# Kernel optimization log

Measured on AMD Instinct MI355X. Metric: run time of the kernel, lower is better.

Reference implementation:

```python
import jax, jax.numpy as jnp
import numpy as np
from jax import lax

B, S, T = 16, 256, 800
V, D, M, H = 256, 512, 80, 1024
NH = 4; HD = D // NH; EH = 256  # encoder LSTM hidden per direction


def setup_inputs() -> dict:
    key = jax.random.key(0)
    it = iter(jax.random.split(key, 40))
    def rn(shape, s=0.05):
        return jax.random.normal(next(it), shape, jnp.float32) * s
    return dict(
        text_inputs=jax.random.randint(next(it), (B, S), 0, V),
        mel_targets=jax.random.normal(next(it), (B, T, M), jnp.float32),
        emb=rn((V, D), 0.1),
        conv_w=rn((3, D, D, 5)), conv_b=rn((3, D)),
        bn_gamma=jnp.ones((3, D)), bn_beta=jnp.zeros((3, D)),
        bn_mean=rn((3, D)), bn_var=jnp.ones((3, D)),
        enc_Wih_f=rn((4 * EH, D)), enc_Whh_f=rn((4 * EH, EH)), enc_b_f=rn((4 * EH,)),
        enc_Wih_b=rn((4 * EH, D)), enc_Whh_b=rn((4 * EH, EH)), enc_b_b=rn((4 * EH,)),
        Wq=rn((D, M)), bq=rn((D,)), Wk=rn((D, D)), bk=rn((D,)),
        Wv=rn((D, D)), bv=rn((D,)), Wo=rn((D, D)), bo=rn((D,)),
        dec_Wih1=rn((4 * H, D + M)), dec_b1=rn((4 * H,)),
        dec_Wih2=rn((4 * H, H)), dec_b2=rn((4 * H,)),
        mel_W=rn((M, H)), mel_b=rn((M,)),
        stop_W=rn((1, H)), stop_b=rn((1,)),
    )


def _lstm_cell_zero(x, Wih, b):
    # single-step LSTM cell from zero (h, c); original resets state every timestep
    g = x @ Wih.T + b
    i, f, gg, o = jnp.split(g, 4, axis=-1)
    c = jax.nn.sigmoid(i) * jnp.tanh(gg)  # c0 = 0 -> forget gate contributes nothing
    return jax.nn.sigmoid(o) * jnp.tanh(c)


def _lstm_scan(xs, Wih, Whh, b, hdim, reverse):
    # xs: (S, B, in); PyTorch gate order i,f,g,o
    def step(carry, xt):
        h, c = carry
        g = xt @ Wih.T + h @ Whh.T + b
        i, f, gg, o = jnp.split(g, 4, axis=-1)
        c = jax.nn.sigmoid(f) * c + jax.nn.sigmoid(i) * jnp.tanh(gg)
        h = jax.nn.sigmoid(o) * jnp.tanh(c)
        return (h, c), h
    z = jnp.zeros((xs.shape[1], hdim), xs.dtype)
    _, hs = lax.scan(step, (z, z), xs, reverse=reverse)
    return hs


def reference(text_inputs, mel_targets, emb, conv_w, conv_b, bn_gamma, bn_beta, bn_mean, bn_var, enc_Wih_f, enc_Whh_f, enc_b_f, enc_Wih_b, enc_Whh_b, enc_b_b, Wq, bq, Wk, bk, Wv, bv, Wo, bo, dec_Wih1, dec_b1, dec_Wih2, dec_b2, mel_W, mel_b, stop_W, stop_b):
    b_, t_, m_ = mel_targets.shape
    # ---- encoder ----
    x = emb[text_inputs].transpose(0, 2, 1)  # (B, D, S)
    for i in range(conv_w.shape[0]):
        x = lax.conv_general_dilated(x, conv_w[i], (1,), [(2, 2)], dimension_numbers=('NCH', 'OIH', 'NCH')) + conv_b[i][None, :, None]
        x = bn_gamma[i][None, :, None] * (x - bn_mean[i][None, :, None]) * lax.rsqrt(bn_var[i][None, :, None] + 1e-5) + bn_beta[i][None, :, None]
        x = jax.nn.relu(x)  # dropout in eval mode -> identity
    xs = x.transpose(2, 0, 1)  # (S, B, D)
    hf = _lstm_scan(xs, enc_Wih_f, enc_Whh_f, enc_b_f, EH, False)
    hb = _lstm_scan(xs, enc_Wih_b, enc_Whh_b, enc_b_b, EH, True)
    enc = jnp.concatenate([hf, hb], -1).transpose(1, 0, 2)  # (B, S, D)
    # ---- decoder (teacher forcing): per-step query = previous mel frame ----
    dec_in = jnp.concatenate([jnp.zeros((b_, 1, m_), mel_targets.dtype), mel_targets[:, :-1]], axis=1)  # (B, T, M)
    q = (dec_in @ Wq.T + bq).reshape(b_, t_, NH, HD)
    k = (enc @ Wk.T + bk).reshape(b_, -1, NH, HD)
    v = (enc @ Wv.T + bv).reshape(b_, -1, NH, HD)
    scores = jnp.einsum('bqhd,bkhd->bhqk', q, k) * (1.0 / np.sqrt(HD)).astype(np.float32)
    attn = jax.nn.softmax(scores, axis=-1)
    ctx = jnp.einsum('bhqk,bkhd->bqhd', attn, v).reshape(b_, t_, D) @ Wo.T + bo
    xcat = jnp.concatenate([ctx, dec_in], axis=-1)  # (B, T, D+M)
    # original re-inits decoder LSTM state each timestep -> stateless per-step cells
    h1 = _lstm_cell_zero(xcat, dec_Wih1, dec_b1)
    h2 = _lstm_cell_zero(h1, dec_Wih2, dec_b2)
    mel = h2 @ mel_W.T + mel_b      # (B, T, 80)
    stop = h2 @ stop_W.T + stop_b   # (B, T, 1) - logits (no sigmoid in training path)
    return mel, stop
```

## Files before the change

kernel.cpp:

```cpp
#include <hip/hip_runtime.h>
#include <hip/hip_bf16.h>
#include <math.h>

#define B_ 16
#define S_ 256
#define T_ 800
#define V_ 256
#define D_ 512
#define M_ 80
#define H_ 1024
#define NH_ 4
#define HD_ 128
#define EH_ 256

using bf16x8 = __attribute__((ext_vector_type(8))) short;
using f32x4  = __attribute__((ext_vector_type(4))) float;
typedef _Float16 half8 __attribute__((ext_vector_type(8)));

__device__ __forceinline__ float sigf(float x) { return 1.f / (1.f + __expf(-x)); }
__device__ __forceinline__ float tanhfast(float x) {
    float e = __expf(2.f * x);
    return 1.f - 2.f / (e + 1.f);
}

__device__ __forceinline__ unsigned short f2bf(float f) {
    unsigned int u = __float_as_uint(f);
    unsigned int r = (u + 0x7FFFu + ((u >> 16) & 1u)) >> 16;
    return (unsigned short)r;
}
__device__ __forceinline__ float bf2f(unsigned short u) {
    return __uint_as_float(((unsigned int)u) << 16);
}
__device__ __forceinline__ unsigned short h2u(_Float16 x) {
    union { _Float16 f; unsigned short u; } c; c.f = x; return c.u;
}

#define LDS_BAR() do {                                        \
    asm volatile("s_waitcnt lgkmcnt(0)" ::: "memory");        \
    __builtin_amdgcn_s_barrier();                             \
    __builtin_amdgcn_sched_barrier(0);                        \
} while (0)

__device__ __forceinline__ void gl_lds16(const unsigned short* g, unsigned short* l) {
    __builtin_amdgcn_global_load_lds((const __attribute__((address_space(1))) void*)g,
                                     (__attribute__((address_space(3))) void*)l, 16, 0, 0);
}

__global__ __launch_bounds__(256) void gemm_mfma(
    const unsigned short* __restrict__ A, const unsigned short* __restrict__ Bw,
    void* __restrict__ Cv, const float* __restrict__ bias,
    int M, int N, int K, int ldc, int epi,
    const float* __restrict__ cb, const float* __restrict__ gam,
    const float* __restrict__ bet, const float* __restrict__ mu,
    const float* __restrict__ va)
{
    __shared__ unsigned short As[4096];
    __shared__ unsigned short Bs[4096];
    const int tid = threadIdx.x, w = tid >> 6, lane = tid & 63;
    const int bm = blockIdx.y * 128, bn = blockIdx.x * 128;
    const int wr = w >> 1, wc = w & 1;

    f32x4 acc[4][4];
#pragma unroll
    for (int m = 0; m < 4; ++m)
#pragma unroll
        for (int n = 0; n < 4; ++n) acc[m][n] = (f32x4){0.f, 0.f, 0.f, 0.f};

    const int r0 = w * 16 + (lane >> 2);
    const int k8 = (lane & 3) * 8;
    const unsigned short* Ag = A + (size_t)(bm + r0) * K + k8;
    const unsigned short* Bg = Bw + (size_t)(bn + r0) * K + k8;
    unsigned short* Al = As + w * 512;
    unsigned short* Bl = Bs + w * 512;

    for (int k0 = 0; k0 < K; k0 += 32) {
        __syncthreads();
        gl_lds16(Ag + k0, Al);
        gl_lds16(Ag + (size_t)64 * K + k0, Al + 2048);
        gl_lds16(Bg + k0, Bl);
        gl_lds16(Bg + (size_t)64 * K + k0, Bl + 2048);
        __syncthreads();
        bf16x8 a[4], b[4];
#pragma unroll
        for (int m = 0; m < 4; ++m)
            a[m] = *(const bf16x8*)(As + (wr * 64 + m * 16 + (lane & 15)) * 32 + (lane >> 4) * 8);
#pragma unroll
        for (int n = 0; n < 4; ++n)
            b[n] = *(const bf16x8*)(Bs + (wc * 64 + n * 16 + (lane & 15)) * 32 + (lane >> 4) * 8);
#pragma unroll
        for (int m = 0; m < 4; ++m)
#pragma unroll
            for (int n = 0; n < 4; ++n)
                acc[m][n] = __builtin_amdgcn_mfma_f32_16x16x32_bf16(a[m], b[n], acc[m][n], 0, 0, 0);
    }

    const int cr = (lane >> 4) * 4, ccol = lane & 15;
#pragma unroll
    for (int m = 0; m < 4; ++m)
#pragma unroll
        for (int n = 0; n < 4; ++n) {
            const int col = bn + wc * 64 + n * 16 + ccol;
            const float bv = (bias && !(epi == 4 && col >= 80)) ? bias[col] : 0.f;
#pragma unroll
            for (int j = 0; j < 4; ++j) {
                const int row = bm + wr * 64 + m * 16 + cr + j;
                float v = acc[m][n][j] + bv;
                if (epi == 1) {
                    float x = v + cb[col];
                    v = fmaxf(0.f, gam[col] * (x - mu[col]) * rsqrtf(va[col] + 1e-5f) + bet[col]);
                }
                if (epi == 2) {
                    ((unsigned short*)Cv)[(size_t)row * ldc + col] = f2bf(v);
                } else if (epi == 3) {
                    const int bb2 = row >> 8, ss = row & 255, hh = col >> 7, dd = col & 127;
                    ((unsigned short*)Cv)[((size_t)(bb2 * 4 + hh) * 128 + dd) * 256 + ss] = f2bf(v);
                } else if (epi == 4) {
                    if (col < 80) ((float*)Cv)[(size_t)row * ldc + col] = v;
                } else {
                    ((float*)Cv)[(size_t)row * ldc + col] = v;
                }
            }
        }
}

__global__ __launch_bounds__(256) void attn_qk(
    const unsigned short* __restrict__ q, const unsigned short* __restrict__ k,
    float* __restrict__ scores)
{
    __shared__ unsigned short As[4096];
    __shared__ unsigned short Bs[4096];
    const int tid = threadIdx.x, w = tid >> 6, lane = tid & 63;
    const int bm = blockIdx.y * 128, bn = blockIdx.x * 128;
    const int z = blockIdx.z, b = z >> 2, h = z & 3;
    const int wr = w >> 1, wc = w & 1;

    const unsigned short* A  = q + ((size_t)b * T_) * 512 + h * 128;
    const unsigned short* Bw = k + ((size_t)b * S_) * 512 + h * 128;

    f32x4 acc[4][4];
#pragma unroll
    for (int m = 0; m < 4; ++m)
#pragma unroll
        for (int n = 0; n < 4; ++n) acc[m][n] = (f32x4){0.f, 0.f, 0.f, 0.f};

    const int r0 = w * 16 + (lane >> 2);
    const int k8 = (lane & 3) * 8;
    const unsigned short* Ag = A + (size_t)(bm + r0) * 512 + k8;
    const unsigned short* Bg = Bw + (size_t)(bn + r0) * 512 + k8;
    unsigned short* Al = As + w * 512;
    unsigned short* Bl = Bs + w * 512;

    for (int k0 = 0; k0 < 128; k0 += 32) {
        __syncthreads();
        gl_lds16(Ag + k0, Al);
        gl_lds16(Ag + (size_t)64 * 512 + k0, Al + 2048);
        gl_lds16(Bg + k0, Bl);
        gl_lds16(Bg + (size_t)64 * 512 + k0, Bl + 2048);
        __syncthreads();
        bf16x8 a[4], bfr[4];
#pragma unroll
        for (int m = 0; m < 4; ++m)
            a[m] = *(const bf16x8*)(As + (wr * 64 + m * 16 + (lane & 15)) * 32 + (lane >> 4) * 8);
#pragma unroll
        for (int n = 0; n < 4; ++n)
            bfr[n] = *(const bf16x8*)(Bs + (wc * 64 + n * 16 + (lane & 15)) * 32 + (lane >> 4) * 8);
#pragma unroll
        for (int m = 0; m < 4; ++m)
#pragma unroll
            for (int n = 0; n < 4; ++n)
                acc[m][n] = __builtin_amdgcn_mfma_f32_16x16x32_bf16(a[m], bfr[n], acc[m][n], 0, 0, 0);
    }

    const int cr = (lane >> 4) * 4, ccol = lane & 15;
#pragma unroll
    for (int m = 0; m < 4; ++m)
#pragma unroll
        for (int n = 0; n < 4; ++n) {
            const int col = bn + wc * 64 + n * 16 + ccol;
#pragma unroll
            for (int j = 0; j < 4; ++j) {
                const int row = bm + wr * 64 + m * 16 + cr + j;
                if (row < T_)
                    scores[((size_t)z * T_ + row) * 256 + col] = acc[m][n][j] * 0.08838834764831843f;
            }
        }
}

__global__ __launch_bounds__(256) void attn_sm(
    const float* __restrict__ scores, unsigned short* __restrict__ probs)
{
    const int row = blockIdx.x * 4 + (threadIdx.x >> 6);
    const int lane = threadIdx.x & 63;
    const float4 v = *(const float4*)(scores + (size_t)row * 256 + lane * 4);
    float m = fmaxf(fmaxf(v.x, v.y), fmaxf(v.z, v.w));
    for (int off = 32; off; off >>= 1) m = fmaxf(m, __shfl_xor(m, off));
    float ex = __expf(v.x - m), ey = __expf(v.y - m), ez = __expf(v.z - m), ew = __expf(v.w - m);
    float sum = ex + ey + ez + ew;
    for (int off = 32; off; off >>= 1) sum += __shfl_xor(sum, off);
    const float inv = 1.f / sum;
    ushort4 o;
    o.x = f2bf(ex * inv); o.y = f2bf(ey * inv); o.z = f2bf(ez * inv); o.w = f2bf(ew * inv);
    *(ushort4*)(probs + (size_t)row * 256 + lane * 4) = o;
}

__global__ __launch_bounds__(256) void attn_pv(
    const unsigned short* __restrict__ probs, const unsigned short* __restrict__ vT,
    unsigned short* __restrict__ ctx)
{
    __shared__ unsigned short As[4096];
    __shared__ unsigned short Bs[4096];
    const int tid = threadIdx.x, w = tid >> 6, lane = tid & 63;
    const int bm = blockIdx.y * 128;
    const int z = blockIdx.z, b = z >> 2, h = z & 3;
    const int wr = w >> 1, wc = w & 1;

    const unsigned short* A  = probs + (size_t)z * T_ * 256;
    const unsigned short* Bw = vT + (size_t)z * 128 * 256;

    f32x4 acc[4][4];
#pragma unroll
    for (int m = 0; m < 4; ++m)
#pragma unroll
        for (int n = 0; n < 4; ++n) acc[m][n] = (f32x4){0.f, 0.f, 0.f, 0.f};

    const int r0 = w * 16 + (lane >> 2);
    const int k8 = (lane & 3) * 8;
    const unsigned short* Ag = A + (size_t)(bm + r0) * 256 + k8;
    const unsigned short* Bg = Bw + (size_t)r0 * 256 + k8;
    unsigned short* Al = As + w * 512;
    unsigned short* Bl = Bs + w * 512;

    for (int k0 = 0; k0 < 256; k0 += 32) {
        __syncthreads();
        gl_lds16(Ag + k0, Al);
        gl_lds16(Ag + (size_t)64 * 256 + k0, Al + 2048);
        gl_lds16(Bg + k0, Bl);
        gl_lds16(Bg + (size_t)64 * 256 + k0, Bl + 2048);
        __syncthreads();
        bf16x8 a[4], bfr[4];
#pragma unroll
        for (int m = 0; m < 4; ++m)
            a[m] = *(const bf16x8*)(As + (wr * 64 + m * 16 + (lane & 15)) * 32 + (lane >> 4) * 8);
#pragma unroll
        for (int n = 0; n < 4; ++n)
            bfr[n] = *(const bf16x8*)(Bs + (wc * 64 + n * 16 + (lane & 15)) * 32 + (lane >> 4) * 8);
#pragma unroll
        for (int m = 0; m < 4; ++m)
#pragma unroll
            for (int n = 0; n < 4; ++n)
                acc[m][n] = __builtin_amdgcn_mfma_f32_16x16x32_bf16(a[m], bfr[n], acc[m][n], 0, 0, 0);
    }

    const int cr = (lane >> 4) * 4, ccol = lane & 15;
#pragma unroll
    for (int m = 0; m < 4; ++m)
#pragma unroll
        for (int n = 0; n < 4; ++n) {
            const int col = wc * 64 + n * 16 + ccol;
#pragma unroll
            for (int j = 0; j < 4; ++j) {
                const int row = bm + wr * 64 + m * 16 + cr + j;
                if (row < T_)
                    ctx[((size_t)b * T_ + row) * 512 + h * 128 + col] = f2bf(acc[m][n][j]);
            }
        }
}

__global__ void embed_k(const int* __restrict__ txt, const float* __restrict__ emb,
                        float* __restrict__ xs)
{
    int idx = blockIdx.x * 256 + threadIdx.x;
    if (idx >= B_ * S_ * D_) return;
    int bs = idx >> 9, dd = idx & 511;
    xs[idx] = emb[(size_t)txt[bs] * D_ + dd];
}

__global__ void im2col_bf(const float* __restrict__ in, unsigned short* __restrict__ out)
{
    int idx = blockIdx.x * 256 + threadIdx.x;
    if (idx >= B_ * S_ * 2560) return;
    int r = idx / 2560, cc = idx % 2560;
    int din = cc / 5, kk = cc % 5;
    int b = r >> 8, s = r & 255;
    int sp = s + kk - 2;
    float v = (sp >= 0 && sp < S_) ? in[((size_t)b * S_ + sp) * D_ + din] : 0.f;
    out[idx] = f2bf(v);
}

__global__ void transp_bf(const float* __restrict__ in, unsigned short* __restrict__ out)
{
    int idx = blockIdx.x * 256 + threadIdx.x;
    if (idx >= B_ * S_ * D_) return;
    int d = idx & 511;
    int sb = idx >> 9;
    int s = sb >> 4, b = sb & 15;
    out[idx] = f2bf(in[((size_t)b * S_ + s) * D_ + d]);
}

__global__ void hist2enc(const _Float16* __restrict__ hist, unsigned short* __restrict__ enc)
{
    int idx = blockIdx.x * 256 + threadIdx.x;
    if (idx >= B_ * S_ * D_) return;
    int d = idx & 511;
    int bs = idx >> 9;
    int b = bs >> 8, s = bs & 255;
    int dir = d >> 8, hid = d & 255;
    enc[idx] = f2bf((float)hist[(((size_t)(dir * 16 + b) * 256 + s) * 256) + hid]);
}

__global__ void cvt_all(
    const float* __restrict__ conv_w, const float* __restrict__ Wih_f,
    const float* __restrict__ Wih_b, const float* __restrict__ Wk,
    const float* __restrict__ Wv, const float* __restrict__ Wq,
    const float* __restrict__ Wo, const float* __restrict__ Wih1,
    const float* __restrict__ Wih2, const float* __restrict__ melW,
    unsigned short* __restrict__ cWc, unsigned short* __restrict__ cWif,
    unsigned short* __restrict__ cWib, unsigned short* __restrict__ cWk,
    unsigned short* __restrict__ cWv, unsigned short* __restrict__ cWq,
    unsigned short* __restrict__ cWo, unsigned short* __restrict__ cW1,
    unsigned short* __restrict__ cW2, unsigned short* __restrict__ cWm)
{
    int idx = blockIdx.x * 256 + threadIdx.x;
    if (idx < 3932160) { cWc[idx] = f2bf(conv_w[idx]); return; }
    idx -= 3932160;
    if (idx < 524288) { cWif[idx] = f2bf(Wih_f[idx]); return; }
    idx -= 524288;
    if (idx < 524288) { cWib[idx] = f2bf(Wih_b[idx]); return; }
    idx -= 524288;
    if (idx < 262144) { cWk[idx] = f2bf(Wk[idx]); return; }
    idx -= 262144;
    if (idx < 262144) { cWv[idx] = f2bf(Wv[idx]); return; }
    idx -= 262144;
    if (idx < 49152) {
        int r = idx / 96, k = idx - r * 96;
        cWq[idx] = (k < 80) ? f2bf(Wq[(size_t)r * 80 + k]) : 0;
        return;
    }
    idx -= 49152;
    if (idx < 262144) { cWo[idx] = f2bf(Wo[idx]); return; }
    idx -= 262144;
    if (idx < 1867776) {
        int n = idx / 608, k = idx - n * 608;
        int orig = (n < 1024) ? n : n + 1024;
        cW1[idx] = (k < 592) ? f2bf(Wih1[(size_t)orig * 592 + k]) : 0;
        return;
    }
    idx -= 1867776;
    if (idx < 3145728) {
        int n = idx >> 10, k = idx & 1023;
        int orig = (n < 1024) ? n : n + 1024;
        cW2[idx] = f2bf(Wih2[(size_t)orig * 1024 + k]);
        return;
    }
    idx -= 3145728;
    if (idx < 131072) {
        int r = idx >> 10, k = idx & 1023;
        cWm[idx] = (r < 80) ? f2bf(melW[(size_t)r * 1024 + k]) : 0;
        return;
    }
}

__global__ void decin_k2(const float* __restrict__ mel, unsigned short* __restrict__ din,
                         unsigned short* __restrict__ xcat)
{
    int idx = blockIdx.x * 256 + threadIdx.x;
    if (idx >= B_ * T_ * 96) return;
    int r = idx / 96, j = idx - r * 96;
    int b = r / T_, t = r - b * T_;
    float v = (j < M_ && t > 0) ? mel[((size_t)b * T_ + t - 1) * M_ + j] : 0.f;
    unsigned short bv = f2bf(v);
    din[(size_t)r * 96 + j] = bv;
    xcat[(size_t)r * 608 + 512 + j] = bv;
}

__global__ void dec_cellb2(const unsigned short* __restrict__ g, const float* __restrict__ b,
                           unsigned short* __restrict__ h, int rows)
{
    int idx = blockIdx.x * 256 + threadIdx.x;
    if (idx >= rows * 512) return;
    int r = idx >> 9, j2 = (idx & 511) * 2;
    const unsigned short* gr = g + (size_t)r * 3072;
    ushort2 vi = *(const ushort2*)(gr + j2);
    ushort2 vg = *(const ushort2*)(gr + 1024 + j2);
    ushort2 vo = *(const ushort2*)(gr + 2048 + j2);
    float i0 = sigf(bf2f(vi.x) + b[j2]),          i1 = sigf(bf2f(vi.y) + b[j2 + 1]);
    float g0 = tanhfast(bf2f(vg.x) + b[2048 + j2]), g1 = tanhfast(bf2f(vg.y) + b[2048 + j2 + 1]);
    float o0 = sigf(bf2f(vo.x) + b[3072 + j2]),   o1 = sigf(bf2f(vo.y) + b[3072 + j2 + 1]);
    ushort2 o;
    o.x = f2bf(o0 * tanhfast(i0 * g0));
    o.y = f2bf(o1 * tanhfast(i1 * g1));
    *(ushort2*)(h + (size_t)r * 1024 + j2) = o;
}

__global__ __launch_bounds__(256) void stop_head(
    const unsigned short* __restrict__ h2, const float* __restrict__ sw,
    const float* __restrict__ sb, float* __restrict__ out)
{
    int row = blockIdx.x * 4 + (threadIdx.x >> 6);
    int lane = threadIdx.x & 63;
    const unsigned short* hr = h2 + (size_t)row * H_;
    float acc = 0.f;
#pragma unroll
    for (int i = 0; i < H_; i += 64) acc += bf2f(hr[i + lane]) * sw[i + lane];
    for (int off = 32; off; off >>= 1) acc += __shfl_xor(acc, off);
    if (lane == 0) out[row] = acc + sb[0];
}

__global__ __launch_bounds__(1024, 4) void lstm_persist8(
    const float* __restrict__ gi_f, const float* __restrict__ gi_b,
    const float* __restrict__ Wf, const float* __restrict__ Wb,
    _Float16* __restrict__ hist,
    unsigned long long* __restrict__ hstage)
{
    const int blk = blockIdx.x;
    const int dir = blk >> 1, half = blk & 1;
    const float* gi = dir ? gi_b : gi_f;
    const float* W  = dir ? Wb : Wf;
    const int tid = threadIdx.x, wid = tid >> 6, lane = tid & 63;
    const int l15 = lane & 15, q = lane >> 4;

    __shared__ _Float16 h_lds[16][264];
    __shared__ float exch[512][17];

    half8 w0[8], w1[8];
    {
        const int gt0 = wid >> 3, hb0 = wid & 7;
        const int gt1 = (wid + 16) >> 3;
        const float* wr0 = W + (size_t)(gt0 * 256 + half * 128 + hb0 * 16 + l15) * 256;
        const float* wr1 = W + (size_t)(gt1 * 256 + half * 128 + hb0 * 16 + l15) * 256;
#pragma unroll
        for (int ks = 0; ks < 8; ++ks) {
            half8 a, b;
#pragma unroll
            for (int j = 0; j < 8; ++j) {
                a[j] = (_Float16)wr0[ks * 32 + q * 8 + j];
                b[j] = (_Float16)wr1[ks * 32 + q * 8 + j];
            }
            w0[ks] = a; w1[ks] = b;
        }
    }
    for (int i = tid; i < 16 * 264; i += 1024) ((_Float16*)h_lds)[i] = (_Float16)0.f;
    for (int i = tid; i < 512 * 17; i += 1024) ((float*)exch)[i] = 0.f;

    const int hid = tid & 127;
    const int ba  = tid >> 7;
    const int bb  = ba + 8;
    const int gh  = half * 128 + hid;
    const int pc  = (half ^ 1) * 128 + hid;
    float c0 = 0.f, c1 = 0.f;

    const int exr0 = (wid >> 3) * 128 + (wid & 7) * 16 + l15;
    const int exr1 = ((wid + 16) >> 3) * 128 + (wid & 7) * 16 + l15;

    const int own_base = ((dir * 2 + half) * 8 + ba) * 128 + hid;
    const int par_base = ((dir * 2 + (half ^ 1)) * 8 + ba) * 128 + hid;

    float gp0[4], gp1[4];
    {
        const int s0 = dir ? 255 : 0;
        const float* g0 = gi + ((size_t)s0 * 16 + ba) * 1024 + gh;
        const float* g1 = gi + ((size_t)s0 * 16 + bb) * 1024 + gh;
#pragma unroll
        for (int g2 = 0; g2 < 4; ++g2) { gp0[g2] = g0[g2 * 256]; gp1[g2] = g1[g2 * 256]; }
    }
    __syncthreads();

    for (int step = 0; step < 255; ++step) {
        const int s = dir ? (255 - step) : step;
        const unsigned int tag = (unsigned int)(step + 1);
        const int slot = (step & 1) * 4096;

        float h0, h1;
        {
            float xi = exch[hid][ba] + gp0[0];
            float xf = exch[128 + hid][ba] + gp0[1];
            float xg = exch[256 + hid][ba] + gp0[2];
            float xo = exch[384 + hid][ba] + gp0[3];
            float ig = sigf(xi), fg = sigf(xf), gg = tanhfast(xg), og = sigf(xo);
            c0 = fg * c0 + ig * gg; h0 = og * tanhfast(c0);
            xi = exch[hid][bb] + gp1[0];
            xf = exch[128 + hid][bb] + gp1[1];
            xg = exch[256 + hid][bb] + gp1[2];
            xo = exch[384 + hid][bb] + gp1[3];
            ig = sigf(xi); fg = sigf(xf); gg = tanhfast(xg); og = sigf(xo);
            c1 = fg * c1 + ig * gg; h1 = og * tanhfast(c1);
        }
        h_lds[ba][gh] = (_Float16)h0;
        h_lds[bb][gh] = (_Float16)h1;
        {
            unsigned int d32 = (unsigned int)h2u((_Float16)h0) |
                               ((unsigned int)h2u((_Float16)h1) << 16);
            unsigned long long wv = ((unsigned long long)tag << 32) | d32;
            __hip_atomic_store(&hstage[slot + own_base], wv,
                               __ATOMIC_RELAXED, __HIP_MEMORY_SCOPE_AGENT);
        }
        hist[(((size_t)(dir * 16 + ba) * 256 + s) * 256) + gh] = (_Float16)h0;
        hist[(((size_t)(dir * 16 + bb) * 256 + s) * 256) + gh] = (_Float16)h1;

        {
            const int s2 = dir ? (254 - step) : (step + 1);
            const float* g0 = gi + ((size_t)s2 * 16 + ba) * 1024 + gh;
            const float* g1 = gi + ((size_t)s2 * 16 + bb) * 1024 + gh;
#pragma unroll
            for (int g2 = 0; g2 < 4; ++g2) { gp0[g2] = g0[g2 * 256]; gp1[g2] = g1[g2 * 256]; }
        }

        {
            unsigned long long pv;
            do {
                pv = __hip_atomic_load(&hstage[slot + par_base],
                                       __ATOMIC_RELAXED, __HIP_MEMORY_SCOPE_AGENT);
            } while ((unsigned int)(pv >> 32) != tag);
            unsigned int d32 = (unsigned int)pv;
            *(unsigned short*)&h_lds[ba][pc] = (unsigned short)(d32 & 0xFFFF);
            *(unsigned short*)&h_lds[bb][pc] = (unsigned short)(d32 >> 16);
        }
        LDS_BAR();

        {
            f32x4 a0 = (f32x4){0.f, 0.f, 0.f, 0.f};
            f32x4 a1 = (f32x4){0.f, 0.f, 0.f, 0.f};
            const _Float16* hrow = &h_lds[l15][0];
#pragma unroll
            for (int ks = 0; ks < 8; ++ks) {
                half8 a = *(const half8*)(hrow + ks * 32 + q * 8);
                a0 = __builtin_amdgcn_mfma_f32_16x16x32_f16(a, w0[ks], a0, 0, 0, 0);
                a1 = __builtin_amdgcn_mfma_f32_16x16x32_f16(a, w1[ks], a1, 0, 0, 0);
            }
            *(f32x4*)&exch[exr0][q * 4] = a0;
            *(f32x4*)&exch[exr1][q * 4] = a1;
        }
        LDS_BAR();
    }

    {
        const int s = dir ? 0 : 255;
        float h0, h1;
        float xi = exch[hid][ba] + gp0[0];
        float xf = exch[128 + hid][ba] + gp0[1];
        float xg = exch[256 + hid][ba] + gp0[2];
        float xo = exch[384 + hid][ba] + gp0[3];
        float ig = sigf(xi), fg = sigf(xf), gg = tanhfast(xg), og = sigf(xo);
        c0 = fg * c0 + ig * gg; h0 = og * tanhfast(c0);
        xi = exch[hid][bb] + gp1[0];
        xf = exch[128 + hid][bb] + gp1[1];
        xg = exch[256 + hid][bb] + gp1[2];
        xo = exch[384 + hid][bb] + gp1[3];
        ig = sigf(xi); fg = sigf(xf); gg = tanhfast(xg); og = sigf(xo);
        c1 = fg * c1 + ig * gg; h1 = og * tanhfast(c1);
        hist[(((size_t)(dir * 16 + ba) * 256 + s) * 256) + gh] = (_Float16)h0;
        hist[(((size_t)(dir * 16 + bb) * 256 + s) * 256) + gh] = (_Float16)h1;
    }
}

static inline void launch_mfma(hipStream_t st, const unsigned short* A, const unsigned short* B,
                               void* C, const float* bias, int M, int N, int K, int ldc, int epi = 0,
                               const float* cb = nullptr, const float* gam = nullptr,
                               const float* bet = nullptr, const float* mu = nullptr,
                               const float* va = nullptr)
{
    dim3 grid(N / 128, M / 128);
    gemm_mfma<<<grid, 256, 0, st>>>(A, B, C, bias, M, N, K, ldc, epi, cb, gam, bet, mu, va);
}

extern "C" void kernel_launch(void* const* d_in, const int* in_sizes, int n_in,
                              void* d_out, int out_size, void* d_ws, size_t ws_size,
                              hipStream_t stream)
{
    const int*   text   = (const int*)d_in[0];
    const float* mel_t  = (const float*)d_in[1];
    const float* emb    = (const float*)d_in[2];
    const float* conv_w = (const float*)d_in[3];
    const float* conv_b = (const float*)d_in[4];
    const float* bn_g   = (const float*)d_in[5];
    const float* bn_b   = (const float*)d_in[6];
    const float* bn_m   = (const float*)d_in[7];
    const float* bn_v   = (const float*)d_in[8];
    const float* Wih_f  = (const float*)d_in[9];
    const float* Whh_f  = (const float*)d_in[10];
    const float* b_f    = (const float*)d_in[11];
    const float* Wih_b  = (const float*)d_in[12];
    const float* Whh_b  = (const float*)d_in[13];
    const float* b_b    = (const float*)d_in[14];
    const float* Wq     = (const float*)d_in[15];
    const float* bq     = (const float*)d_in[16];
    const float* Wk     = (const float*)d_in[17];
    const float* bk     = (const float*)d_in[18];
    const float* Wv     = (const float*)d_in[19];
    const float* bv     = (const float*)d_in[20];
    const float* Wo     = (const float*)d_in[21];
    const float* bo     = (const float*)d_in[22];
    const float* Wih1   = (const float*)d_in[23];
    const float* b1     = (const float*)d_in[24];
    const float* Wih2   = (const float*)d_in[25];
    const float* b2     = (const float*)d_in[26];
    const float* melW   = (const float*)d_in[27];
    const float* melb   = (const float*)d_in[28];
    const float* stopW  = (const float*)d_in[29];
    const float* stopb  = (const float*)d_in[30];
    float* out = (float*)d_out;
    (void)in_sizes; (void)n_in; (void)out_size; (void)ws_size;

    float* ws = (float*)d_ws;
    float* big  = ws;
    float* pool = ws + 13107200;

    unsigned long long* hstage = (unsigned long long*)(ws + 6000000);

    float*          gi_f   = pool + 0;
    float*          gi_b   = pool + 4194304;
    unsigned short* enc_bf = (unsigned short*)(pool + 8388608);
    float*          P0     = pool + 9437184;
    float*          P1     = pool + 11534336;
    unsigned short* xsT    = (unsigned short*)(pool + 13631488);
    _Float16*       hist   = (_Float16*)(pool + 14155776);
    unsigned short* kbf    = (unsigned short*)(pool + 0);
    unsigned short* vT     = (unsigned short*)(pool + 1048576);
    unsigned short* qbf    = (unsigned short*)(pool + 2097152);
    unsigned short* probs  = (unsigned short*)(pool + 9437184);
    unsigned short* dinb   = (unsigned short*)(pool + 16008192);
    unsigned short* ctxb   = (unsigned short*)(pool + 16622592);
    unsigned short* gatesb = (unsigned short*)(pool + 0);
    unsigned short* h2b    = (unsigned short*)big;
    unsigned short* h1b    = (unsigned short*)(big + 4000000);
    unsigned short* xcat   = (unsigned short*)(pool + 19899392);
    float*          WB     = pool + 23790592;
    unsigned short* cWc  = (unsigned short*)(WB + 0);
    unsigned short* cWif = (unsigned short*)(WB + 1966080);
    unsigned short* cWib = (unsigned short*)(WB + 2228224);
    unsigned short* cWk  = (unsigned short*)(WB + 2490368);
    unsigned short* cWv  = (unsigned short*)(WB + 2621440);
    unsigned short* cWq  = (unsigned short*)(WB + 2752512);
    unsigned short* cWo  = (unsigned short*)(WB + 2777088);
    unsigned short* cW1  = (unsigned short*)(WB + 2908160);
    unsigned short* cW2  = (unsigned short*)(WB + 3842048);
    unsigned short* cWm  = (unsigned short*)(WB + 5414912);

    auto ceil256 = [](int n) { return (n + 255) / 256; };

    hipMemsetAsync(hstage, 0, 8192 * 8, stream);

    cvt_all<<<ceil256(10960896), 256, 0, stream>>>(
        conv_w, Wih_f, Wih_b, Wk, Wv, Wq, Wo, Wih1, Wih2, melW,
        cWc, cWif, cWib, cWk, cWv, cWq, cWo, cW1, cW2, cWm);

    embed_k<<<ceil256(B_ * S_ * D_), 256, 0, stream>>>(text, emb, P0);
    float* cin = P0;
    float* cout = P1;
    for (int l = 0; l < 3; ++l) {
        im2col_bf<<<ceil256(B_ * S_ * 2560), 256, 0, stream>>>(cin, (unsigned short*)big);
        launch_mfma(stream, (unsigned short*)big, cWc + (size_t)l * 512 * 2560,
                    cout, nullptr, B_ * S_, 512, 2560, 512, 1,
                    conv_b + l * 512, bn_g + l * 512, bn_b + l * 512, bn_m + l * 512, bn_v + l * 512);
        float* tmp = cin; cin = cout; cout = tmp;
    }
    transp_bf<<<ceil256(B_ * S_ * D_), 256, 0, stream>>>(cin, xsT);

    launch_mfma(stream, xsT, cWif, gi_f, b_f, S_ * B_, 1024, 512, 1024);
    launch_mfma(stream, xsT, cWib, gi_b, b_b, S_ * B_, 1024, 512, 1024);
    lstm_persist8<<<4, 1024, 0, stream>>>(gi_f, gi_b, Whh_f, Whh_b, hist, hstage);
    hist2enc<<<ceil256(B_ * S_ * D_), 256, 0, stream>>>(hist, enc_bf);

    launch_mfma(stream, enc_bf, cWk, kbf, bk, B_ * S_, 512, 512, 512, 2);
    launch_mfma(stream, enc_bf, cWv, vT, bv, B_ * S_, 512, 512, 0, 3);
    decin_k2<<<ceil256(B_ * T_ * 96), 256, 0, stream>>>(mel_t, dinb, xcat);
    launch_mfma(stream, dinb, cWq, qbf, bq, B_ * T_, 512, 96, 512, 2);

    attn_qk<<<dim3(2, 7, 64), 256, 0, stream>>>(qbf, kbf, big);
    attn_sm<<<12800, 256, 0, stream>>>(big, probs);
    attn_pv<<<dim3(1, 7, 64), 256, 0, stream>>>(probs, vT, ctxb);

    launch_mfma(stream, ctxb, cWo, xcat, bo, B_ * T_, 512, 512, 608, 2);

    launch_mfma(stream, xcat, cW1, gatesb, nullptr, B_ * T_, 3072, 608, 3072, 2);
    dec_cellb2<<<ceil256(B_ * T_ * 512), 256, 0, stream>>>(gatesb, b1, h1b, B_ * T_);
    launch_mfma(stream, h1b, cW2, gatesb, nullptr, B_ * T_, 3072, 1024, 3072, 2);
    dec_cellb2<<<ceil256(B_ * T_ * 512), 256, 0, stream>>>(gatesb, b2, h2b, B_ * T_);

    launch_mfma(stream, h2b, cWm, out, melb, B_ * T_, 128, 1024, 80, 4);
    stop_head<<<(B_ * T_) / 4, 256, 0, stream>>>(h2b, stopW, stopb, out + (size_t)B_ * T_ * M_);
}
```

Baseline: 1.622 ms.

## Fuse attention QK with softmax and split LSTM recurrence to overlap peer exchange

The QK score kernel and the separate softmax kernel become one kernel. Each block owns 64 query rows across all 256 keys and does the row max and sum in registers plus a small LDS reduction, so the fp32 score matrix is never written to or read back from global memory. Separately, the persistent encoder LSTM splits its recurrent matmul into a local-half part and a peer-half part. The local-half MFMAs run before spinning on the peer block's hidden-state exchange, which is meant to hide inter-block latency on the serial critical path, at the cost of an extra barrier per step.

New measurement: 1.576 ms. 1.03x faster.

```diff
diff --git a/kernel.cpp b/kernel.cpp
--- a/kernel.cpp
+++ b/kernel.cpp
@@ -34,12 +34,6 @@
 __device__ __forceinline__ unsigned short h2u(_Float16 x) {
     union { _Float16 f; unsigned short u; } c; c.f = x; return c.u;
 }
-
-#define LDS_BAR() do {                                        \
-    asm volatile("s_waitcnt lgkmcnt(0)" ::: "memory");        \
-    __builtin_amdgcn_s_barrier();                             \
-    __builtin_amdgcn_sched_barrier(0);                        \
-} while (0)
 
 __device__ __forceinline__ void gl_lds16(const unsigned short* g, unsigned short* l) {
     __builtin_amdgcn_global_load_lds((const __attribute__((address_space(1))) void*)g,
@@ -123,16 +117,18 @@
         }
 }
 
-__global__ __launch_bounds__(256) void attn_qk(
+__global__ __launch_bounds__(256) void attn_qksm(
     const unsigned short* __restrict__ q, const unsigned short* __restrict__ k,
-    float* __restrict__ scores)
-{
-    __shared__ unsigned short As[4096];
-    __shared__ unsigned short Bs[4096];
-    const int tid = threadIdx.x, w = tid >> 6, lane = tid & 63;
-    const int bm = blockIdx.y * 128, bn = blockIdx.x * 128;
-    const int z = blockIdx.z, b = z >> 2, h = z & 3;
-    const int wr = w >> 1, wc = w & 1;
+    unsigned short* __restrict__ probs)
+{
+    __shared__ unsigned short As[2048];
+    __shared__ unsigned short Bs[8192];
+    __shared__ float redm[64][4];
+    __shared__ float reds[64][4];
+    const int tid = threadIdx.x, wid = tid >> 6, lane = tid & 63;
+    const int l15 = lane & 15, bq = lane >> 4;
+    const int bm = blockIdx.x * 64;
+    const int z = blockIdx.y, b = z >> 2, h = z & 3;
 
     const unsigned short* A  = q + ((size_t)b * T_) * 512 + h * 128;
     const unsigned short* Bw = k + ((size_t)b * S_) * 512 + h * 128;
@@ -143,64 +139,81 @@
 #pragma unroll
         for (int n = 0; n < 4; ++n) acc[m][n] = (f32x4){0.f, 0.f, 0.f, 0.f};
 
-    const int r0 = w * 16 + (lane >> 2);
+    const int r0 = wid * 16 + (lane >> 2);
     const int k8 = (lane & 3) * 8;
-    const unsigned short* Ag = A + (size_t)(bm + r0) * 512 + k8;
-    const unsigned short* Bg = Bw + (size_t)(bn + r0) * 512 + k8;
-    unsigned short* Al = As + w * 512;
-    unsigned short* Bl = Bs + w * 512;
 
     for (int k0 = 0; k0 < 128; k0 += 32) {
         __syncthreads();
-        gl_lds16(Ag + k0, Al);
-        gl_lds16(Ag + (size_t)64 * 512 + k0, Al + 2048);
-        gl_lds16(Bg + k0, Bl);
-        gl_lds16(Bg + (size_t)64 * 512 + k0, Bl + 2048);
+        gl_lds16(A + (size_t)(bm + r0) * 512 + k0 + k8, As + wid * 512);
+        gl_lds16(Bw + (size_t)r0 * 512 + k0 + k8,          Bs + wid * 512);
+        gl_lds16(Bw + (size_t)(64 + r0) * 512 + k0 + k8,   Bs + 2048 + wid * 512);
+        gl_lds16(Bw + (size_t)(128 + r0) * 512 + k0 + k8,  Bs + 4096 + wid * 512);
+        gl_lds16(Bw + (size_t)(192 + r0) * 512 + k0 + k8,  Bs + 6144 + wid * 512);
         __syncthreads();
-        bf16x8 a[4], bfr[4];
+        bf16x8 a[4], bb[4];
 #pragma unroll
         for (int m = 0; m < 4; ++m)
-            a[m] = *(const bf16x8*)(As + (wr * 64 + m * 16 + (lane & 15)) * 32 + (lane >> 4) * 8);
+            a[m] = *(const bf16x8*)(As + (m * 16 + l15) * 32 + bq * 8);
 #pragma unroll
         for (int n = 0; n < 4; ++n)
-            bfr[n] = *(const bf16x8*)(Bs + (wc * 64 + n * 16 + (lane & 15)) * 32 + (lane >> 4) * 8);
+            bb[n] = *(const bf16x8*)(Bs + (wid * 64 + n * 16 + l15) * 32 + bq * 8);
 #pragma unroll
         for (int m = 0; m < 4; ++m)
 #pragma unroll
             for (int n = 0; n < 4; ++n)
-                acc[m][n] = __builtin_amdgcn_mfma_f32_16x16x32_bf16(a[m], bfr[n], acc[m][n], 0, 0, 0);
+                acc[m][n] = __builtin_amdgcn_mfma_f32_16x16x32_bf16(a[m], bb[n], acc[m][n], 0, 0, 0);
     }
 
     const int cr = (lane >> 4) * 4, ccol = lane & 15;
-#pragma unroll
-    for (int m = 0; m < 4; ++m)
-#pragma unroll
-        for (int n = 0; n < 4; ++n) {
-            const int col = bn + wc * 64 + n * 16 + ccol;
-#pragma unroll
-            for (int j = 0; j < 4; ++j) {
-                const int row = bm + wr * 64 + m * 16 + cr + j;
-                if (row < T_)
-                    scores[((size_t)z * T_ + row) * 256 + col] = acc[m][n][j] * 0.08838834764831843f;
+    const float SC = 0.08838834764831843f;
+
+    float lmax[4][4];
+#pragma unroll
+    for (int m = 0; m < 4; ++m)
+#pragma unroll
+        for (int j = 0; j < 4; ++j) {
+            float v = fmaxf(fmaxf(acc[m][0][j], acc[m][1][j]),
+                            fmaxf(acc[m][2][j], acc[m][3][j]));
+#pragma unroll
+            for (int off = 1; off < 16; off <<= 1) v = fmaxf(v, __shfl_xor(v, off));
+            lmax[m][j] = v;
+            if (ccol == 0) redm[m * 16 + cr + j][wid] = v;
+        }
+    __syncthreads();
+    float lsum[4][4];
+#pragma unroll
+    for (int m = 0; m < 4; ++m)
+#pragma unroll
+        for (int j = 0; j < 4; ++j) {
+            const int r = m * 16 + cr + j;
+            float mx = fmaxf(fmaxf(redm[r][0], redm[r][1]), fmaxf(redm[r][2], redm[r][3]));
+            lmax[m][j] = mx;
+            float s = 0.f;
+#pragma unroll
+            for (int n = 0; n < 4; ++n) {
+                float p = __expf((acc[m][n][j] - mx) * SC);
+                acc[m][n][j] = p;
+                s += p;
             }
-        }
-}
-
-__global__ __launch_bounds__(256) void attn_sm(
-    const float* __restrict__ scores, unsigned short* __restrict__ probs)
-{
-    const int row = blockIdx.x * 4 + (threadIdx.x >> 6);
-    const int lane = threadIdx.x & 63;
-    const float4 v = *(const float4*)(scores + (size_t)row * 256 + lane * 4);
-    float m = fmaxf(fmaxf(v.x, v.y), fmaxf(v.z, v.w));
-    for (int off = 32; off; off >>= 1) m = fmaxf(m, __shfl_xor(m, off));
-    float ex = __expf(v.x - m), ey = __expf(v.y - m), ez = __expf(v.z - m), ew = __expf(v.w - m);
-    float sum = ex + ey + ez + ew;
-    for (int off = 32; off; off >>= 1) sum += __shfl_xor(sum, off);
-    const float inv = 1.f / sum;
-    ushort4 o;
-    o.x = f2bf(ex * inv); o.y = f2bf(ey * inv); o.z = f2bf(ez * inv); o.w = f2bf(ew * inv);
-    *(ushort4*)(probs + (size_t)row * 256 + lane * 4) = o;
+#pragma unroll
+            for (int off = 1; off < 16; off <<= 1) s += __shfl_xor(s, off);
+            lsum[m][j] = s;
+            if (ccol == 0) reds[r][wid] = s;
+        }
+    __syncthreads();
+#pragma unroll
+    for (int m = 0; m < 4; ++m)
+#pragma unroll
+        for (int j = 0; j < 4; ++j) {
+            const int r = m * 16 + cr + j;
+            const int row = bm + r;
+            if (row >= T_) continue;
+            const float inv = 1.f / (reds[r][0] + reds[r][1] + reds[r][2] + reds[r][3]);
+#pragma unroll
+            for (int n = 0; n < 4; ++n)
+                probs[((size_t)z * T_ + row) * 256 + wid * 64 + n * 16 + ccol] =
+                    f2bf(acc[m][n][j] * inv);
+        }
 }
 
 __global__ __launch_bounds__(256) void attn_pv(
@@ -406,7 +419,7 @@
     if (lane == 0) out[row] = acc + sb[0];
 }
 
-__global__ __launch_bounds__(1024, 4) void lstm_persist8(
+__global__ __launch_bounds__(1024, 4) void lstm_persist9(
     const float* __restrict__ gi_f, const float* __restrict__ gi_b,
     const float* __restrict__ Wf, const float* __restrict__ Wb,
     _Float16* __restrict__ hist,
@@ -418,25 +431,30 @@
     const float* W  = dir ? Wb : Wf;
     const int tid = threadIdx.x, wid = tid >> 6, lane = tid & 63;
     const int l15 = lane & 15, q = lane >> 4;
+    const int half4 = half * 4, ph4 = (half ^ 1) * 4;
 
     __shared__ _Float16 h_lds[16][264];
     __shared__ float exch[512][17];
 
-    half8 w0[8], w1[8];
+    half8 wOA[4], wPA[4], wOB[4], wPB[4];
     {
         const int gt0 = wid >> 3, hb0 = wid & 7;
         const int gt1 = (wid + 16) >> 3;
         const float* wr0 = W + (size_t)(gt0 * 256 + half * 128 + hb0 * 16 + l15) * 256;
         const float* wr1 = W + (size_t)(gt1 * 256 + half * 128 + hb0 * 16 + l15) * 256;
 #pragma unroll
-        for (int ks = 0; ks < 8; ++ks) {
-            half8 a, b;
+        for (int i = 0; i < 4; ++i) {
+            const int kO = (half4 + i) * 32 + q * 8;
+            const int kP = (ph4 + i) * 32 + q * 8;
+            half8 a, b, c, d;
 #pragma unroll
             for (int j = 0; j < 8; ++j) {
-                a[j] = (_Float16)wr0[ks * 32 + q * 8 + j];
-                b[j] = (_Float16)wr1[ks * 32 + q * 8 + j];
+                a[j] = (_Float16)wr0[kO + j];
+                b[j] = (_Float16)wr0[kP + j];
+                c[j] = (_Float16)wr1[kO + j];
+                d[j] = (_Float16)wr1[kP + j];
             }
-            w0[ks] = a; w1[ks] = b;
+            wOA[i] = a; wPA[i] = b; wOB[i] = c; wPB[i] = d;
         }
     }
     for (int i = tid; i < 16 * 264; i += 1024) ((_Float16*)h_lds)[i] = (_Float16)0.f;
@@ -465,7 +483,7 @@
     }
     __syncthreads();
 
-    for (int step = 0; step < 255; ++step) {
+    for (int step = 0; step < 256; ++step) {
         const int s = dir ? (255 - step) : step;
         const unsigned int tag = (unsigned int)(step + 1);
         const int slot = (step & 1) * 4096;
@@ -485,8 +503,6 @@
             ig = sigf(xi); fg = sigf(xf); gg = tanhfast(xg); og = sigf(xo);
             c1 = fg * c1 + ig * gg; h1 = og * tanhfast(c1);
         }
-        h_lds[ba][gh] = (_Float16)h0;
-        h_lds[bb][gh] = (_Float16)h1;
         {
             unsigned int d32 = (unsigned int)h2u((_Float16)h0) |
                                ((unsigned int)h2u((_Float16)h1) << 16);
@@ -494,62 +510,50 @@
             __hip_atomic_store(&hstage[slot + own_base], wv,
                                __ATOMIC_RELAXED, __HIP_MEMORY_SCOPE_AGENT);
         }
+        h_lds[ba][gh] = (_Float16)h0;
+        h_lds[bb][gh] = (_Float16)h1;
         hist[(((size_t)(dir * 16 + ba) * 256 + s) * 256) + gh] = (_Float16)h0;
         hist[(((size_t)(dir * 16 + bb) * 256 + s) * 256) + gh] = (_Float16)h1;
-
-        {
+        if (step < 255) {
             const int s2 = dir ? (254 - step) : (step + 1);
             const float* g0 = gi + ((size_t)s2 * 16 + ba) * 1024 + gh;
             const float* g1 = gi + ((size_t)s2 * 16 + bb) * 1024 + gh;
 #pragma unroll
             for (int g2 = 0; g2 < 4; ++g2) { gp0[g2] = g0[g2 * 256]; gp1[g2] = g1[g2 * 256]; }
         }
-
-        {
-            unsigned long long pv;
-            do {
-                pv = __hip_atomic_load(&hstage[slot + par_base],
-                                       __ATOMIC_RELAXED, __HIP_MEMORY_SCOPE_AGENT);
-            } while ((unsigned int)(pv >> 32) != tag);
-            unsigned int d32 = (unsigned int)pv;
-            *(unsigned short*)&h_lds[ba][pc] = (unsigned short)(d32 & 0xFFFF);
-            *(unsigned short*)&h_lds[bb][pc] = (unsigned short)(d32 >> 16);
-        }
-        LDS_BAR();
-
-        {
-            f32x4 a0 = (f32x4){0.f, 0.f, 0.f, 0.f};
-            f32x4 a1 = (f32x4){0.f, 0.f, 0.f, 0.f};
+        __syncthreads();
+
+        if (step < 255) {
+            f32x4 acc0 = (f32x4){0.f, 0.f, 0.f, 0.f};
+            f32x4 acc1 = (f32x4){0.f, 0.f, 0.f, 0.f};
             const _Float16* hrow = &h_lds[l15][0];
 #pragma unroll
-            for (int ks = 0; ks < 8; ++ks) {
-                half8 a = *(const half8*)(hrow + ks * 32 + q * 8);
-                a0 = __builtin_amdgcn_mfma_f32_16x16x32_f16(a, w0[ks], a0, 0, 0, 0);
-                a1 = __builtin_amdgcn_mfma_f32_16x16x32_f16(a, w1[ks], a1, 0, 0, 0);
+            for (int i = 0; i < 4; ++i) {
+                half8 a = *(const half8*)(hrow + (half4 + i) * 32 + q * 8);
+                acc0 = __builtin_amdgcn_mfma_f32_16x16x32_f16(a, wOA[i], acc0, 0, 0, 0);
+                acc1 = __builtin_amdgcn_mfma_f32_16x16x32_f16(a, wOB[i], acc1, 0, 0, 0);
             }
-            *(f32x4*)&exch[exr0][q * 4] = a0;
-            *(f32x4*)&exch[exr1][q * 4] = a1;
-        }
-        LDS_BAR();
-    }
-
-    {
-        const int s = dir ? 0 : 255;
-        float h0, h1;
-        float xi = exch[hid][ba] + gp0[0];
-        float xf = exch[128 + hid][ba] + gp0[1];
-        float xg = exch[256 + hid][ba] + gp0[2];
-        float xo = exch[384 + hid][ba] + gp0[3];
-        float ig = sigf(xi), fg = sigf(xf), gg = tanhfast(xg), og = sigf(xo);
-        c0 = fg * c0 + ig * gg; h0 = og * tanhfast(c0);
-        xi = exch[hid][bb] + gp1[0];
-        xf = exch[128 + hid][bb] + gp1[1];
-        xg = exch[256 + hid][bb] + gp1[2];
-        xo = exch[384 + hid][bb] + gp1[3];
-        ig = sigf(xi); fg = sigf(xf); gg = tanhfast(xg); og = sigf(xo);
-        c1 = fg * c1 + ig * gg; h1 = og * tanhfast(c1);
-        hist[(((size_t)(dir * 16 + ba) * 256 + s) * 256) + gh] = (_Float16)h0;
-        hist[(((size_t)(dir * 16 + bb) * 256 + s) * 256) + gh] = (_Float16)h1;
+            {
+                unsigned long long pv;
+                do {
+                    pv = __hip_atomic_load(&hstage[slot + par_base],
+                                           __ATOMIC_RELAXED, __HIP_MEMORY_SCOPE_AGENT);
+                } while ((unsigned int)(pv >> 32) != tag);
+                unsigned int d32 = (unsigned int)pv;
+                *(unsigned short*)&h_lds[ba][pc] = (unsigned short)(d32 & 0xFFFF);
+                *(unsigned short*)&h_lds[bb][pc] = (unsigned short)(d32 >> 16);
+            }
+            __syncthreads();
+#pragma unroll
+            for (int i = 0; i < 4; ++i) {
+                half8 a = *(const half8*)(hrow + (ph4 + i) * 32 + q * 8);
+                acc0 = __builtin_amdgcn_mfma_f32_16x16x32_f16(a, wPA[i], acc0, 0, 0, 0);
+                acc1 = __builtin_amdgcn_mfma_f32_16x16x32_f16(a, wPB[i], acc1, 0, 0, 0);
+            }
+            *(f32x4*)&exch[exr0][q * 4] = acc0;
+            *(f32x4*)&exch[exr1][q * 4] = acc1;
+            __syncthreads();
+        }
     }
 }
 
@@ -658,7 +662,7 @@
 
     launch_mfma(stream, xsT, cWif, gi_f, b_f, S_ * B_, 1024, 512, 1024);
     launch_mfma(stream, xsT, cWib, gi_b, b_b, S_ * B_, 1024, 512, 1024);
-    lstm_persist8<<<4, 1024, 0, stream>>>(gi_f, gi_b, Whh_f, Whh_b, hist, hstage);
+    lstm_persist9<<<4, 1024, 0, stream>>>(gi_f, gi_b, Whh_f, Whh_b, hist, hstage);
     hist2enc<<<ceil256(B_ * S_ * D_), 256, 0, stream>>>(hist, enc_bf);
 
     launch_mfma(stream, enc_bf, cWk, kbf, bk, B_ * S_, 512, 512, 512, 2);
@@ -666,8 +670,7 @@
     decin_k2<<<ceil256(B_ * T_ * 96), 256, 0, stream>>>(mel_t, dinb, xcat);
     launch_mfma(stream, dinb, cWq, qbf, bq, B_ * T_, 512, 96, 512, 2);
 
-    attn_qk<<<dim3(2, 7, 64), 256, 0, stream>>>(qbf, kbf, big);
-    attn_sm<<<12800, 256, 0, stream>>>(big, probs);
+    attn_qksm<<<dim3(13, 64), 256, 0, stream>>>(qbf, kbf, probs);
     attn_pv<<<dim3(1, 7, 64), 256, 0, stream>>>(probs, vT, ctxb);
 
     launch_mfma(stream, ctxb, cWo, xcat, bo, B_ * T_, 512, 512, 608, 2);
```
